# Performance work log

Measured on AMD Instinct MI355X. Metric: run time of the kernel, lower is better.

Reference implementation:

```python
import jax, jax.numpy as jnp
import numpy as np

B, S, E, H = 4, 2048, 1024, 16
D = E // H
EPS = 1e-6


def setup_inputs() -> dict:
    key = jax.random.key(0)
    ks = jax.random.split(key, 6)
    glorot = lambda k: jax.random.uniform(k, (E, E), jnp.float32,
                                          -np.sqrt(6.0 / (E + E)), np.sqrt(6.0 / (E + E)))
    return {
        "x": jax.random.normal(ks[0], (B, S, E), jnp.float32),
        "mask": jnp.zeros((B, 1, 1, S), jnp.float32),
        "Wq": glorot(ks[1]), "bq": jnp.zeros((E,), jnp.float32),
        "Wk": glorot(ks[2]), "bk": jnp.zeros((E,), jnp.float32),
        "Wv": glorot(ks[3]), "bv": jnp.zeros((E,), jnp.float32),
        "Wo": glorot(ks[4]), "bo": jnp.zeros((E,), jnp.float32),
        "gamma": jnp.ones((E,), jnp.float32),
        "beta": jnp.zeros((E,), jnp.float32),
    }


def _split_heads(t):
    # [B, S, E] -> [B, H, S, D]
    return t.reshape(B, S, H, D).transpose(0, 2, 1, 3)


def reference(x, mask, Wq, bq, Wk, bk, Wv, bv, Wo, bo, gamma, beta):
    q = _split_heads(x @ Wq + bq)
    k = _split_heads(x @ Wk + bk)
    v = _split_heads(x @ Wv + bv)
    # NOTE: original divides by sqrt(embedding_size), not sqrt(depth)
    scores = jnp.einsum("bhqd,bhkd->bhqk", q, k) / jnp.sqrt(jnp.float32(E))
    scores = scores + mask * (-1e9)
    attn = jax.nn.softmax(scores, axis=-1)
    ctx = jnp.einsum("bhqk,bhkd->bhqd", attn, v)
    ctx = ctx.transpose(0, 2, 1, 3).reshape(B, S, E)
    main_out = ctx @ Wo + bo
    # dropout is identity (is_training=False); residual is the raw input
    added = main_out + x
    mu = jnp.mean(added, axis=-1, keepdims=True)
    var = jnp.mean(jnp.square(added - mu), axis=-1, keepdims=True)
    return gamma * (added - mu) / jnp.sqrt(var + EPS) + beta
```

## Files before the change

### kernel.cpp

```cpp
#include <hip/hip_runtime.h>
#include <hip/hip_bf16.h>


typedef __bf16 bf16_t;
typedef __bf16 bf16x8 __attribute__((ext_vector_type(8)));
typedef __bf16 bf16x4v __attribute__((ext_vector_type(4)));
typedef float f32x4 __attribute__((ext_vector_type(4)));

#define LDS_AS __attribute__((address_space(3)))
#define GLB_AS __attribute__((address_space(1)))

__device__ __forceinline__ void async16(bf16_t* lds, const bf16_t* g) {
  __builtin_amdgcn_global_load_lds((GLB_AS void*)const_cast<bf16_t*>(g),
                                   (LDS_AS void*)lds, 16, 0, 0);
}

__device__ __forceinline__ f32x4 mfma16(bf16x8 a, bf16x8 b, f32x4 c) {
  return __builtin_amdgcn_mfma_f32_16x16x32_bf16(a, b, c, 0, 0, 0);
}

__device__ __forceinline__ float fast_exp2(float x) {
#if __has_builtin(__builtin_amdgcn_exp2f)
  return __builtin_amdgcn_exp2f(x);
#else
  return __expf(x * 0.6931471805599453f);
#endif
}

__global__ __launch_bounds__(256) void prep_k(
    const float* __restrict__ w0, const float* __restrict__ w1,
    const float* __restrict__ w2, const float* __restrict__ w3,
    bf16_t* __restrict__ dst,
    const float* __restrict__ x, bf16_t* __restrict__ xb)
{
  const int tx = threadIdx.x, ty = threadIdx.y;
  if (blockIdx.z == 4) {
    const int id = (blockIdx.y * 32 + blockIdx.x) * 256 + ty * 32 + tx;
#pragma unroll
    for (int it = 0; it < 8; ++it) {
      const size_t i = ((size_t)id + (size_t)it * 262144) * 4;
      const float4 v = *(const float4*)(x + i);
      bf16x4v o;
      o[0] = (bf16_t)v.x; o[1] = (bf16_t)v.y; o[2] = (bf16_t)v.z; o[3] = (bf16_t)v.w;
      *(bf16x4v*)(xb + i) = o;
    }
    return;
  }
  __shared__ bf16_t tile[32][33];
  const float* src = (blockIdx.z == 0) ? w0 : (blockIdx.z == 1) ? w1
                   : (blockIdx.z == 2) ? w2 : w3;
  bf16_t* d = dst + (size_t)blockIdx.z * 1024 * 1024;
  const int bx = blockIdx.x * 32, by = blockIdx.y * 32;
#pragma unroll
  for (int r = 0; r < 32; r += 8)
    tile[ty + r][tx] = (bf16_t)src[(size_t)(by + ty + r) * 1024 + bx + tx];
  __syncthreads();
#pragma unroll
  for (int r = 0; r < 32; r += 8)
    d[(size_t)(bx + ty + r) * 1024 + by + tx] = tile[tx][ty + r];
}

__global__ __launch_bounds__(256) void gemm_qkv(
    const bf16_t* __restrict__ X, const bf16_t* __restrict__ WtAll,
    const float* __restrict__ bq, const float* __restrict__ bk,
    const float* __restrict__ bv,
    bf16_t* __restrict__ Qb, bf16_t* __restrict__ Kb, bf16_t* __restrict__ Vtb)
{
  __shared__ __align__(16) bf16_t As[128 * 64];
  __shared__ __align__(16) bf16_t Bs[128 * 64];

  const int z = blockIdx.z;
  const bf16_t* Bt = WtAll + (size_t)z * 1024 * 1024;
  const float* bias = (z == 0) ? bq : (z == 1) ? bk : bv;
  const int bm0 = blockIdx.x * 128;
  const int bn0 = blockIdx.y * 128;
  const int t = threadIdx.x;
  const int w = t >> 6, lane = t & 63;
  const int wm = w >> 1, wn = w & 1;
  const int l15 = lane & 15, quad = lane >> 4;
  const int srow8 = lane >> 3;
  const int sp8   = lane & 7;

  f32x4 acc[4][4] = {};

  for (int k0 = 0; k0 < 1024; k0 += 64) {
    __syncthreads();
#pragma unroll
    for (int i = 0; i < 4; ++i) {
      const int row = (w * 4 + i) * 8 + srow8;
      const int c = sp8 ^ (row & 7);
      async16(&As[row * 64 + sp8 * 8], X  + (size_t)(bm0 + row) * 1024 + k0 + c * 8);
      async16(&Bs[row * 64 + sp8 * 8], Bt + (size_t)(bn0 + row) * 1024 + k0 + c * 8);
    }
    __syncthreads();

    bf16x8 af[4][2], bfr[4][2];
#pragma unroll
    for (int mi = 0; mi < 4; ++mi) {
      const int r = wm * 64 + mi * 16 + l15;
#pragma unroll
      for (int kc = 0; kc < 2; ++kc) {
        const int pg = (kc * 4 + quad) ^ (r & 7);
        af[mi][kc] = *(const bf16x8*)&As[r * 64 + pg * 8];
      }
    }
#pragma unroll
    for (int ni = 0; ni < 4; ++ni) {
      const int r = wn * 64 + ni * 16 + l15;
#pragma unroll
      for (int kc = 0; kc < 2; ++kc) {
        const int pg = (kc * 4 + quad) ^ (r & 7);
        bfr[ni][kc] = *(const bf16x8*)&Bs[r * 64 + pg * 8];
      }
    }
#pragma unroll
    for (int kc = 0; kc < 2; ++kc)
#pragma unroll
      for (int mi = 0; mi < 4; ++mi)
#pragma unroll
        for (int ni = 0; ni < 4; ++ni)
          acc[mi][ni] = mfma16(af[mi][kc], bfr[ni][kc], acc[mi][ni]);
  }

  const float QSCALE = 0.045084220f;

#pragma unroll
  for (int ni = 0; ni < 4; ++ni) {
    const int n = bn0 + wn * 64 + ni * 16 + l15;
    const float bb = bias[n];
    const int h = n >> 6, dd = n & 63;
    if (z == 2) {
#pragma unroll
      for (int mi = 0; mi < 4; ++mi) {
        const int m0 = bm0 + wm * 64 + mi * 16 + quad * 4;
        const int bi = m0 >> 11, s = m0 & 2047;
        bf16x4v vk;
#pragma unroll
        for (int r = 0; r < 4; ++r) vk[r] = (bf16_t)(acc[mi][ni][r] + bb);
        *(bf16x4v*)&Vtb[((size_t)(bi * 16 + h) * 64 + dd) * 2048 + s] = vk;
      }
    } else {
#pragma unroll
      for (int mi = 0; mi < 4; ++mi) {
#pragma unroll
        for (int r = 0; r < 4; ++r) {
          const int m = bm0 + wm * 64 + mi * 16 + quad * 4 + r;
          const float v = acc[mi][ni][r] + bb;
          const int bi = m >> 11, s = m & 2047;
          if (z == 0)
            Qb[((size_t)(bi * 16 + h) * 2048 + s) * 64 + dd] = (bf16_t)(v * QSCALE);
          else
            Kb[((size_t)(bi * 16 + h) * 2048 + s) * 64 + dd] = (bf16_t)v;
        }
      }
    }
  }
}

__global__ __launch_bounds__(256, 4) void attn_k(
    const bf16_t* __restrict__ Qb, const bf16_t* __restrict__ Kb,
    const bf16_t* __restrict__ Vtb, const float* __restrict__ mask,
    bf16_t* __restrict__ Ctx)
{
  __shared__ __align__(16) bf16_t Ks[64 * 64];
  __shared__ __align__(16) bf16_t Vs[64 * 64];
  __shared__ __align__(16) bf16_t Ps[256 * 64];
  __shared__ __align__(16) float maskv[64];

  const int lin = blockIdx.y * 8 + blockIdx.x;
  const int qt = lin >> 6;
  const int bh = (lin & 7) * 8 + ((lin >> 3) & 7);
  const int bi = bh >> 4, h = bh & 15;
  const int q0 = qt * 256;
  const bf16_t* Qh = Qb + (size_t)bh * 2048 * 64;
  const bf16_t* Kh = Kb + (size_t)bh * 2048 * 64;
  const bf16_t* Vh = Vtb + (size_t)bh * 64 * 2048;

  const int t = threadIdx.x;
  const int w = t >> 6, lane = t & 63;
  const int l15 = lane & 15, quad = lane >> 4;

  bf16x8 qb[4][2];
#pragma unroll
  for (int ni = 0; ni < 4; ++ni)
#pragma unroll
    for (int kc = 0; kc < 2; ++kc)
      qb[ni][kc] = *(const bf16x8*)&Qh[(size_t)(q0 + w * 64 + ni * 16 + l15) * 64
                                       + kc * 32 + quad * 8];

  bf16x8 ones;
#pragma unroll
  for (int i = 0; i < 8; ++i) ones[i] = (bf16_t)1.0f;

  f32x4 oacc[4][4] = {};
  f32x4 lacc[4] = {};

  const int srow = lane >> 3;
  const int sp = lane & 7;

  for (int j = 0; j < 32; ++j) {
    const int k0 = j * 64;
    __syncthreads();
#pragma unroll
    for (int i = 0; i < 2; ++i) {
      const int row = (w * 2 + i) * 8 + srow;
      const int c = sp ^ (row & 7);
      async16(&Ks[row * 64 + sp * 8], Kh + (size_t)(k0 + row) * 64 + c * 8);
      async16(&Vs[row * 64 + sp * 8], Vh + (size_t)row * 2048 + k0 + c * 8);
    }
    if (t < 64) maskv[t] = mask[bi * 2048 + k0 + t] * (-1.442695e9f);
    __syncthreads();

    f32x4 sacc[4][4];
#pragma unroll
    for (int mi = 0; mi < 4; ++mi) {
      const float4 mk = *(const float4*)&maskv[mi * 16 + quad * 4];
      f32x4 cinit; cinit[0] = mk.x; cinit[1] = mk.y; cinit[2] = mk.z; cinit[3] = mk.w;
#pragma unroll
      for (int ni = 0; ni < 4; ++ni) sacc[mi][ni] = cinit;
    }
#pragma unroll
    for (int mi = 0; mi < 4; ++mi) {
      const int r = mi * 16 + l15;
      const bf16x8 kf0 = *(const bf16x8*)&Ks[r * 64 + ((0 * 4 + quad) ^ (r & 7)) * 8];
      const bf16x8 kf1 = *(const bf16x8*)&Ks[r * 64 + ((1 * 4 + quad) ^ (r & 7)) * 8];
#pragma unroll
      for (int ni = 0; ni < 4; ++ni) {
        sacc[mi][ni] = mfma16(kf0, qb[ni][0], sacc[mi][ni]);
        sacc[mi][ni] = mfma16(kf1, qb[ni][1], sacc[mi][ni]);
      }
    }

#pragma unroll
    for (int ni = 0; ni < 4; ++ni) {
      const int row = w * 64 + ni * 16 + l15;
#pragma unroll
      for (int mi = 0; mi < 4; ++mi) {
        bf16x4v pk;
        pk[0] = (bf16_t)fast_exp2(sacc[mi][ni][0]);
        pk[1] = (bf16_t)fast_exp2(sacc[mi][ni][1]);
        pk[2] = (bf16_t)fast_exp2(sacc[mi][ni][2]);
        pk[3] = (bf16_t)fast_exp2(sacc[mi][ni][3]);
        const int pg = (mi * 2 + (quad >> 1)) ^ (row & 7);
        *(bf16x4v*)&Ps[row * 64 + pg * 8 + (quad & 1) * 4] = pk;
      }
    }

    bf16x8 pb[4][2];
#pragma unroll
    for (int ni = 0; ni < 4; ++ni)
#pragma unroll
      for (int kc = 0; kc < 2; ++kc) {
        const int row = w * 64 + ni * 16 + l15;
        const int pg = (kc * 4 + quad) ^ (row & 7);
        pb[ni][kc] = *(const bf16x8*)&Ps[row * 64 + pg * 8];
      }
#pragma unroll
    for (int mi = 0; mi < 4; ++mi) {
      const int r = mi * 16 + l15;
      const bf16x8 av0 = *(const bf16x8*)&Vs[r * 64 + ((0 * 4 + quad) ^ (r & 7)) * 8];
      const bf16x8 av1 = *(const bf16x8*)&Vs[r * 64 + ((1 * 4 + quad) ^ (r & 7)) * 8];
#pragma unroll
      for (int ni = 0; ni < 4; ++ni) {
        oacc[mi][ni] = mfma16(av0, pb[ni][0], oacc[mi][ni]);
        oacc[mi][ni] = mfma16(av1, pb[ni][1], oacc[mi][ni]);
      }
    }
#pragma unroll
    for (int ni = 0; ni < 4; ++ni) {
      lacc[ni] = mfma16(ones, pb[ni][0], lacc[ni]);
      lacc[ni] = mfma16(ones, pb[ni][1], lacc[ni]);
    }
  }

#pragma unroll
  for (int ni = 0; ni < 4; ++ni) {
    const float inv = 1.0f / lacc[ni][0];
    const int s = q0 + w * 64 + ni * 16 + l15;
#pragma unroll
    for (int mi = 0; mi < 4; ++mi) {
      bf16x4v o4;
      o4[0] = (bf16_t)(oacc[mi][ni][0] * inv);
      o4[1] = (bf16_t)(oacc[mi][ni][1] * inv);
      o4[2] = (bf16_t)(oacc[mi][ni][2] * inv);
      o4[3] = (bf16_t)(oacc[mi][ni][3] * inv);
      *(bf16x4v*)&Ctx[((size_t)bi * 2048 + s) * 1024 + h * 64 + mi * 16 + quad * 4] = o4;
    }
  }
}

__global__ __launch_bounds__(256) void gemm_proj(
    const bf16_t* __restrict__ Ctx, const bf16_t* __restrict__ WoT,
    const float* __restrict__ bo, const float* __restrict__ Xres,
    float* __restrict__ Add)
{
  __shared__ __align__(16) bf16_t As[128 * 64];
  __shared__ __align__(16) bf16_t Bs[128 * 64];

  const int bm0 = blockIdx.x * 128;
  const int bn0 = blockIdx.y * 128;
  const int t = threadIdx.x;
  const int w = t >> 6, lane = t & 63;
  const int wm = w >> 1, wn = w & 1;
  const int l15 = lane & 15, quad = lane >> 4;
  const int srow8 = lane >> 3;
  const int sp8   = lane & 7;

  f32x4 acc[4][4] = {};

  for (int k0 = 0; k0 < 1024; k0 += 64) {
    __syncthreads();
#pragma unroll
    for (int i = 0; i < 4; ++i) {
      const int row = (w * 4 + i) * 8 + srow8;
      const int c = sp8 ^ (row & 7);
      async16(&As[row * 64 + sp8 * 8], Ctx + (size_t)(bm0 + row) * 1024 + k0 + c * 8);
      async16(&Bs[row * 64 + sp8 * 8], WoT + (size_t)(bn0 + row) * 1024 + k0 + c * 8);
    }
    __syncthreads();

    bf16x8 af[4][2], bfr[4][2];
#pragma unroll
    for (int mi = 0; mi < 4; ++mi) {
      const int r = wm * 64 + mi * 16 + l15;
#pragma unroll
      for (int kc = 0; kc < 2; ++kc) {
        const int pg = (kc * 4 + quad) ^ (r & 7);
        af[mi][kc] = *(const bf16x8*)&As[r * 64 + pg * 8];
      }
    }
#pragma unroll
    for (int ni = 0; ni < 4; ++ni) {
      const int r = wn * 64 + ni * 16 + l15;
#pragma unroll
      for (int kc = 0; kc < 2; ++kc) {
        const int pg = (kc * 4 + quad) ^ (r & 7);
        bfr[ni][kc] = *(const bf16x8*)&Bs[r * 64 + pg * 8];
      }
    }
#pragma unroll
    for (int kc = 0; kc < 2; ++kc)
#pragma unroll
      for (int mi = 0; mi < 4; ++mi)
#pragma unroll
        for (int ni = 0; ni < 4; ++ni)
          acc[mi][ni] = mfma16(af[mi][kc], bfr[ni][kc], acc[mi][ni]);
  }

#pragma unroll
  for (int ni = 0; ni < 4; ++ni) {
    const int n = bn0 + wn * 64 + ni * 16 + l15;
    const float bb = bo[n];
#pragma unroll
    for (int mi = 0; mi < 4; ++mi) {
#pragma unroll
      for (int r = 0; r < 4; ++r) {
        const int m = bm0 + wm * 64 + mi * 16 + quad * 4 + r;
        Add[(size_t)m * 1024 + n] =
            acc[mi][ni][r] + bb + Xres[(size_t)m * 1024 + n];
      }
    }
  }
}

__global__ __launch_bounds__(256) void ln_k(
    const float* __restrict__ A, const float* __restrict__ gamma,
    const float* __restrict__ beta, float* __restrict__ out)
{
  const int wid = threadIdx.x >> 6, lane = threadIdx.x & 63;
  const int row = blockIdx.x * 4 + wid;
  const float* a = A + (size_t)row * 1024;

  float4 v[4];
#pragma unroll
  for (int k = 0; k < 4; ++k) v[k] = ((const float4*)a)[lane + k * 64];

  float s = 0.f;
#pragma unroll
  for (int k = 0; k < 4; ++k) s += (v[k].x + v[k].y) + (v[k].z + v[k].w);
#pragma unroll
  for (int o = 1; o < 64; o <<= 1) s += __shfl_xor(s, o);
  const float mu = s * (1.0f / 1024.0f);

  float q = 0.f;
#pragma unroll
  for (int k = 0; k < 4; ++k) {
    v[k].x -= mu; v[k].y -= mu; v[k].z -= mu; v[k].w -= mu;
    q += (v[k].x * v[k].x + v[k].y * v[k].y) + (v[k].z * v[k].z + v[k].w * v[k].w);
  }
#pragma unroll
  for (int o = 1; o < 64; o <<= 1) q += __shfl_xor(q, o);
  const float rs = rsqrtf(q * (1.0f / 1024.0f) + 1e-6f);

#pragma unroll
  for (int k = 0; k < 4; ++k) {
    const int c = lane + k * 64;
    const float4 g4 = ((const float4*)gamma)[c];
    const float4 b4 = ((const float4*)beta)[c];
    float4 o4;
    o4.x = g4.x * v[k].x * rs + b4.x;
    o4.y = g4.y * v[k].y * rs + b4.y;
    o4.z = g4.z * v[k].z * rs + b4.z;
    o4.w = g4.w * v[k].w * rs + b4.w;
    ((float4*)(out + (size_t)row * 1024))[c] = o4;
  }
}

extern "C" void kernel_launch(void* const* d_in, const int* in_sizes, int n_in,
                              void* d_out, int out_size, void* d_ws, size_t ws_size,
                              hipStream_t stream)
{
  const float* x     = (const float*)d_in[0];
  const float* mask  = (const float*)d_in[1];
  const float* Wq    = (const float*)d_in[2];
  const float* bq    = (const float*)d_in[3];
  const float* Wk    = (const float*)d_in[4];
  const float* bk    = (const float*)d_in[5];
  const float* Wv    = (const float*)d_in[6];
  const float* bv    = (const float*)d_in[7];
  const float* Wo    = (const float*)d_in[8];
  const float* bo    = (const float*)d_in[9];
  const float* gamma = (const float*)d_in[10];
  const float* beta  = (const float*)d_in[11];
  float* out = (float*)d_out;

  bf16_t* Wt  = (bf16_t*)d_ws;
  bf16_t* Xb  = Wt + (size_t)4 * 1024 * 1024;
  bf16_t* Qb  = Xb + (size_t)8192 * 1024;
  bf16_t* Kb  = Qb + (size_t)8192 * 1024;
  bf16_t* Vtb = Kb + (size_t)8192 * 1024;
  bf16_t* Ctx = Vtb + (size_t)8192 * 1024;
  float*  Add = (float*)(Ctx + (size_t)8192 * 1024);

  prep_k<<<dim3(32, 32, 5), dim3(32, 8), 0, stream>>>(Wq, Wk, Wv, Wo, Wt, x, Xb);
  gemm_qkv<<<dim3(64, 8, 3), 256, 0, stream>>>(Xb, Wt, bq, bk, bv, Qb, Kb, Vtb);
  attn_k<<<dim3(8, 64), 256, 0, stream>>>(Qb, Kb, Vtb, mask, Ctx);
  gemm_proj<<<dim3(64, 8), 256, 0, stream>>>(Ctx, Wt + (size_t)3 * 1024 * 1024, bo, x, Add);
  ln_k<<<2048, 256, 0, stream>>>(Add, gamma, beta, out);
}
```

Before: 303.0 us.

## Split attention key range across two wave groups with LDS reduction

The attention kernel now uses 512 threads per block. Two groups of four waves each process half of the key sequence for the same 256 queries, with separate K/V LDS buffers, and their partial outputs and row sums are combined through LDS at the end. The P staging is also cut to per-wave 64x32 chunks processed in two halves, which shrinks LDS and register pressure. This trades extra reduction traffic and a larger block for twice as many waves in flight to hide latency. The fixed-max softmax stays valid because no max subtraction is done.

```diff
diff --git a/kernel.cpp b/kernel.cpp
--- a/kernel.cpp
+++ b/kernel.cpp
@@ -157,15 +157,16 @@
   }
 }
 
-__global__ __launch_bounds__(256, 4) void attn_k(
+__global__ __launch_bounds__(512, 4) void attn_k(
     const bf16_t* __restrict__ Qb, const bf16_t* __restrict__ Kb,
     const bf16_t* __restrict__ Vtb, const float* __restrict__ mask,
     bf16_t* __restrict__ Ctx)
 {
-  __shared__ __align__(16) bf16_t Ks[64 * 64];
-  __shared__ __align__(16) bf16_t Vs[64 * 64];
-  __shared__ __align__(16) bf16_t Ps[256 * 64];
-  __shared__ __align__(16) float maskv[64];
+  __shared__ __align__(16) bf16_t Ks[2][64 * 64];
+  __shared__ __align__(16) bf16_t Vs[2][64 * 64];
+  __shared__ __align__(16) bf16_t Ps[8][64 * 32];
+  __shared__ __align__(16) float maskv[128];
+  __shared__ __align__(16) float Lcom[4][64][4];
 
   const int lin = blockIdx.y * 8 + blockIdx.x;
   const int qt = lin >> 6;
@@ -178,14 +179,21 @@
 
   const int t = threadIdx.x;
   const int w = t >> 6, lane = t & 63;
+  const int g = w >> 2;
+  const int wg = w & 3;
   const int l15 = lane & 15, quad = lane >> 4;
+  const int srow = lane >> 3;
+  const int sp = lane & 7;
+
+  const bf16_t* Kh_g = Kh + (size_t)g * 1024 * 64;
+  const bf16_t* Vh_g = Vh + g * 1024;
 
   bf16x8 qb[4][2];
 #pragma unroll
   for (int ni = 0; ni < 4; ++ni)
 #pragma unroll
     for (int kc = 0; kc < 2; ++kc)
-      qb[ni][kc] = *(const bf16x8*)&Qh[(size_t)(q0 + w * 64 + ni * 16 + l15) * 64
+      qb[ni][kc] = *(const bf16x8*)&Qh[(size_t)(q0 + wg * 64 + ni * 16 + l15) * 64
                                        + kc * 32 + quad * 8];
 
   bf16x8 ones;
@@ -195,26 +203,26 @@
   f32x4 oacc[4][4] = {};
   f32x4 lacc[4] = {};
 
-  const int srow = lane >> 3;
-  const int sp = lane & 7;
-
-  for (int j = 0; j < 32; ++j) {
+  bf16_t* Pw = &Ps[w][0];
+
+  for (int j = 0; j < 16; ++j) {
     const int k0 = j * 64;
     __syncthreads();
 #pragma unroll
     for (int i = 0; i < 2; ++i) {
-      const int row = (w * 2 + i) * 8 + srow;
+      const int row = (wg * 2 + i) * 8 + srow;
       const int c = sp ^ (row & 7);
-      async16(&Ks[row * 64 + sp * 8], Kh + (size_t)(k0 + row) * 64 + c * 8);
-      async16(&Vs[row * 64 + sp * 8], Vh + (size_t)row * 2048 + k0 + c * 8);
-    }
-    if (t < 64) maskv[t] = mask[bi * 2048 + k0 + t] * (-1.442695e9f);
+      async16(&Ks[g][row * 64 + sp * 8], Kh_g + (size_t)(k0 + row) * 64 + c * 8);
+      async16(&Vs[g][row * 64 + sp * 8], Vh_g + (size_t)row * 2048 + k0 + c * 8);
+    }
+    if (t < 128)
+      maskv[t] = mask[bi * 2048 + (t >> 6) * 1024 + k0 + (t & 63)] * (-1.442695e9f);
     __syncthreads();
 
     f32x4 sacc[4][4];
 #pragma unroll
     for (int mi = 0; mi < 4; ++mi) {
-      const float4 mk = *(const float4*)&maskv[mi * 16 + quad * 4];
+      const float4 mk = *(const float4*)&maskv[g * 64 + mi * 16 + quad * 4];
       f32x4 cinit; cinit[0] = mk.x; cinit[1] = mk.y; cinit[2] = mk.z; cinit[3] = mk.w;
 #pragma unroll
       for (int ni = 0; ni < 4; ++ni) sacc[mi][ni] = cinit;
@@ -222,8 +230,8 @@
 #pragma unroll
     for (int mi = 0; mi < 4; ++mi) {
       const int r = mi * 16 + l15;
-      const bf16x8 kf0 = *(const bf16x8*)&Ks[r * 64 + ((0 * 4 + quad) ^ (r & 7)) * 8];
-      const bf16x8 kf1 = *(const bf16x8*)&Ks[r * 64 + ((1 * 4 + quad) ^ (r & 7)) * 8];
+      const bf16x8 kf0 = *(const bf16x8*)&Ks[g][r * 64 + ((0 * 4 + quad) ^ (r & 7)) * 8];
+      const bf16x8 kf1 = *(const bf16x8*)&Ks[g][r * 64 + ((1 * 4 + quad) ^ (r & 7)) * 8];
 #pragma unroll
       for (int ni = 0; ni < 4; ++ni) {
         sacc[mi][ni] = mfma16(kf0, qb[ni][0], sacc[mi][ni]);
@@ -232,59 +240,88 @@
     }
 
 #pragma unroll
+    for (int kc = 0; kc < 2; ++kc) {
+#pragma unroll
+      for (int ni = 0; ni < 4; ++ni) {
+        const int row = ni * 16 + l15;
+#pragma unroll
+        for (int mi2 = 0; mi2 < 2; ++mi2) {
+          const f32x4 sv = sacc[kc * 2 + mi2][ni];
+          bf16x4v pk;
+          pk[0] = (bf16_t)fast_exp2(sv[0]);
+          pk[1] = (bf16_t)fast_exp2(sv[1]);
+          pk[2] = (bf16_t)fast_exp2(sv[2]);
+          pk[3] = (bf16_t)fast_exp2(sv[3]);
+          const int pg = (mi2 * 2 + (quad >> 1)) ^ (row & 3);
+          *(bf16x4v*)&Pw[row * 32 + pg * 8 + (quad & 1) * 4] = pk;
+        }
+      }
+      bf16x8 pb[4];
+#pragma unroll
+      for (int ni = 0; ni < 4; ++ni) {
+        const int row = ni * 16 + l15;
+        const int gi = quad ^ (row & 3);
+        pb[ni] = *(const bf16x8*)&Pw[row * 32 + gi * 8];
+      }
+#pragma unroll
+      for (int mi = 0; mi < 4; ++mi) {
+        const int r = mi * 16 + l15;
+        const bf16x8 av = *(const bf16x8*)&Vs[g][r * 64 + ((kc * 4 + quad) ^ (r & 7)) * 8];
+#pragma unroll
+        for (int ni = 0; ni < 4; ++ni)
+          oacc[mi][ni] = mfma16(av, pb[ni], oacc[mi][ni]);
+      }
+#pragma unroll
+      for (int ni = 0; ni < 4; ++ni)
+        lacc[ni] = mfma16(ones, pb[ni], lacc[ni]);
+    }
+  }
+
+  float* Com = (float*)&Ps[0][0];
+#pragma unroll
+  for (int c = 0; c < 2; ++c) {
+    __syncthreads();
+    if (w >= 4) {
+      const int jb = w - 4;
+#pragma unroll
+      for (int p = 0; p < 2; ++p)
+#pragma unroll
+        for (int ni = 0; ni < 4; ++ni)
+          *(f32x4*)&Com[(((jb * 2 + p) * 4 + ni) * 64 + lane) * 4] = oacc[c * 2 + p][ni];
+      if (c == 0) {
+#pragma unroll
+        for (int ni = 0; ni < 4; ++ni) Lcom[jb][lane][ni] = lacc[ni][0];
+      }
+    }
+    __syncthreads();
+    if (w < 4) {
+#pragma unroll
+      for (int p = 0; p < 2; ++p)
+#pragma unroll
+        for (int ni = 0; ni < 4; ++ni) {
+          const f32x4 o = *(const f32x4*)&Com[(((w * 2 + p) * 4 + ni) * 64 + lane) * 4];
+          oacc[c * 2 + p][ni][0] += o[0];
+          oacc[c * 2 + p][ni][1] += o[1];
+          oacc[c * 2 + p][ni][2] += o[2];
+          oacc[c * 2 + p][ni][3] += o[3];
+        }
+    }
+  }
+
+  if (w < 4) {
+#pragma unroll
     for (int ni = 0; ni < 4; ++ni) {
-      const int row = w * 64 + ni * 16 + l15;
+      const float inv = 1.0f / (lacc[ni][0] + Lcom[w][lane][ni]);
+      const int s = q0 + wg * 64 + ni * 16 + l15;
 #pragma unroll
       for (int mi = 0; mi < 4; ++mi) {
-        bf16x4v pk;
-        pk[0] = (bf16_t)fast_exp2(sacc[mi][ni][0]);
-        pk[1] = (bf16_t)fast_exp2(sacc[mi][ni][1]);
-        pk[2] = (bf16_t)fast_exp2(sacc[mi][ni][2]);
-        pk[3] = (bf16_t)fast_exp2(sacc[mi][ni][3]);
-        const int pg = (mi * 2 + (quad >> 1)) ^ (row & 7);
-        *(bf16x4v*)&Ps[row * 64 + pg * 8 + (quad & 1) * 4] = pk;
-      }
-    }
-
-    bf16x8 pb[4][2];
-#pragma unroll
-    for (int ni = 0; ni < 4; ++ni)
-#pragma unroll
-      for (int kc = 0; kc < 2; ++kc) {
-        const int row = w * 64 + ni * 16 + l15;
-        const int pg = (kc * 4 + quad) ^ (row & 7);
-        pb[ni][kc] = *(const bf16x8*)&Ps[row * 64 + pg * 8];
-      }
-#pragma unroll
-    for (int mi = 0; mi < 4; ++mi) {
-      const int r = mi * 16 + l15;
-      const bf16x8 av0 = *(const bf16x8*)&Vs[r * 64 + ((0 * 4 + quad) ^ (r & 7)) * 8];
-      const bf16x8 av1 = *(const bf16x8*)&Vs[r * 64 + ((1 * 4 + quad) ^ (r & 7)) * 8];
-#pragma unroll
-      for (int ni = 0; ni < 4; ++ni) {
-        oacc[mi][ni] = mfma16(av0, pb[ni][0], oacc[mi][ni]);
-        oacc[mi][ni] = mfma16(av1, pb[ni][1], oacc[mi][ni]);
-      }
-    }
-#pragma unroll
-    for (int ni = 0; ni < 4; ++ni) {
-      lacc[ni] = mfma16(ones, pb[ni][0], lacc[ni]);
-      lacc[ni] = mfma16(ones, pb[ni][1], lacc[ni]);
-    }
-  }
-
-#pragma unroll
-  for (int ni = 0; ni < 4; ++ni) {
-    const float inv = 1.0f / lacc[ni][0];
-    const int s = q0 + w * 64 + ni * 16 + l15;
-#pragma unroll
-    for (int mi = 0; mi < 4; ++mi) {
-      bf16x4v o4;
-      o4[0] = (bf16_t)(oacc[mi][ni][0] * inv);
-      o4[1] = (bf16_t)(oacc[mi][ni][1] * inv);
-      o4[2] = (bf16_t)(oacc[mi][ni][2] * inv);
-      o4[3] = (bf16_t)(oacc[mi][ni][3] * inv);
-      *(bf16x4v*)&Ctx[((size_t)bi * 2048 + s) * 1024 + h * 64 + mi * 16 + quad * 4] = o4;
+        bf16x4v o4;
+        o4[0] = (bf16_t)(oacc[mi][ni][0] * inv);
+        o4[1] = (bf16_t)(oacc[mi][ni][1] * inv);
+        o4[2] = (bf16_t)(oacc[mi][ni][2] * inv);
+        o4[3] = (bf16_t)(oacc[mi][ni][3] * inv);
+        *(bf16x4v*)&Ctx[((size_t)bi * 2048 + s) * 1024 + h * 64 + mi * 16 + quad * 4] = o4;
+      }
     }
   }
 }
@@ -434,7 +471,7 @@
 
   prep_k<<<dim3(32, 32, 5), dim3(32, 8), 0, stream>>>(Wq, Wk, Wv, Wo, Wt, x, Xb);
   gemm_qkv<<<dim3(64, 8, 3), 256, 0, stream>>>(Xb, Wt, bq, bk, bv, Qb, Kb, Vtb);
-  attn_k<<<dim3(8, 64), 256, 0, stream>>>(Qb, Kb, Vtb, mask, Ctx);
+  attn_k<<<dim3(8, 64), 512, 0, stream>>>(Qb, Kb, Vtb, mask, Ctx);
   gemm_proj<<<dim3(64, 8), 256, 0, stream>>>(Ctx, Wt + (size_t)3 * 1024 * 1024, bo, x, Add);
   ln_k<<<2048, 256, 0, stream>>>(Add, gamma, beta, out);
 }
```

Measured after the change: 733.1 us. +142.0%, slower.
